# Kernel optimization log

Measured on AMD Instinct MI355X. Metric: run time of the kernel, lower is better.

## Reference

```python
import jax, jax.numpy as jnp
import numpy as np

NEG_SLOPE = 0.2  # HANConv default negative_slope
N_NODES = 100000
N_REL = 8
N_EDGES = 200000
N_LABEL = 131072
C_IN = 128
H1 = 128
H2 = 128


def _segment_softmax(logits, seg, num_segments):
    # PyG softmax(src, index): exp(src - max_per_seg) / (sum_per_seg + 1e-16)
    m = jax.ops.segment_max(logits, seg, num_segments=num_segments)
    m = jnp.where(jnp.isfinite(m), m, 0.0)  # empty segments -> 0
    e = jnp.exp(logits - m[seg])
    s = jax.ops.segment_sum(e, seg, num_segments=num_segments)
    return e / (s[seg] + 1e-16)


def _han_layer(x, edge_index, proj_w, proj_b, att_src, att_dst, q, klin_w, klin_b):
    # x: [N, Cin]; edge_index: [R, 2, E]; att_src/att_dst: [R, D]; klin_w: [D, D] (torch [out,in])
    N = x.shape[0]
    h = x @ proj_w + proj_b            # [N, D] shared projection for node type 'node'
    a_src = h @ att_src.T              # [N, R] per-node src attention logits
    a_dst = h @ att_dst.T              # [N, R]

    def per_rel(eidx, a_s, a_d):
        src, dst = eidx[0], eidx[1]
        alpha = jax.nn.leaky_relu(a_s[src] + a_d[dst], NEG_SLOPE)     # [E]
        alpha = _segment_softmax(alpha, dst, N)                        # softmax over in-neighbors
        out = jax.ops.segment_sum(alpha[:, None] * h[src], dst, num_segments=N)  # [N, D]
        return jax.nn.relu(out)        # HANConv applies relu per edge-type output

    outs = jax.vmap(per_rel, in_axes=(0, 1, 1))(edge_index, a_src, a_dst)  # [R, N, D]
    # semantic attention across edge types (group())
    score = jnp.einsum('d,rd->r', q, jnp.tanh(outs @ klin_w.T + klin_b).mean(axis=1))
    attn = jax.nn.softmax(score)       # [R]
    return jnp.einsum('r,rnd->nd', attn, outs)


def setup_inputs() -> dict:
    key = jax.random.key(0)
    ks = jax.random.split(key, 24)
    f32 = jnp.float32

    def lin_w(k, fin, fout):
        return (jax.random.normal(k, (fin, fout), f32) / np.sqrt(fin)).astype(f32)

    inp = {
        'x': jax.random.normal(ks[0], (N_NODES, C_IN), f32),
        'edge_index': jax.random.randint(ks[1], (N_REL, 2, N_EDGES), 0, N_NODES, jnp.int32),
        'edge_label_index': jax.random.randint(ks[2], (2, N_LABEL), 0, N_NODES, jnp.int32),
        # HANConv layer 1 params
        'w1': lin_w(ks[3], C_IN, H1), 'b1': jnp.zeros((H1,), f32),
        'asrc1': jax.random.normal(ks[4], (N_REL, H1), f32) / np.sqrt(H1),
        'adst1': jax.random.normal(ks[5], (N_REL, H1), f32) / np.sqrt(H1),
        'q1': jax.random.normal(ks[6], (H1,), f32) / np.sqrt(H1),
        'kw1': lin_w(ks[7], H1, H1).T, 'kb1': jnp.zeros((H1,), f32),
        # HANConv layer 2 params
        'w2': lin_w(ks[8], H1, H2), 'b2': jnp.zeros((H2,), f32),
        'asrc2': jax.random.normal(ks[9], (N_REL, H2), f32) / np.sqrt(H2),
        'adst2': jax.random.normal(ks[10], (N_REL, H2), f32) / np.sqrt(H2),
        'q2': jax.random.normal(ks[11], (H2,), f32) / np.sqrt(H2),
        'kw2': lin_w(ks[12], H2, H2).T, 'kb2': jnp.zeros((H2,), f32),
        # link-score head
        'post_w': lin_w(ks[13], H2, 2), 'post_b': jnp.zeros((2,), f32),
    }
    return inp


def reference(x, edge_index, edge_label_index,
              w1, b1, asrc1, adst1, q1, kw1, kb1,
              w2, b2, asrc2, adst2, q2, kw2, kb2,
              post_w, post_b):
    h = jax.nn.relu(_han_layer(x, edge_index, w1, b1, asrc1, adst1, q1, kw1, kb1))
    h = jax.nn.relu(_han_layer(h, edge_index, w2, b2, asrc2, adst2, q2, kw2, kb2))
    h_had = h[edge_label_index[0]] * h[edge_label_index[1]]   # [L, H2]
    logits = h_had @ post_w + post_b                          # [L, 2]
    return logits.sum(axis=-1)                                # [L]
```

## Files before the change

kernel.cpp:

```cpp
#include <hip/hip_runtime.h>

#define NN 100000
#define NR 8
#define NE 200000
#define NL 131072
#define NSEG (NR*NN)
#define NB_SCAN 782
#define NPAD (NB_SCAN*1024)

typedef __attribute__((ext_vector_type(8))) short short8;
typedef __attribute__((ext_vector_type(4))) float floatx4;

__device__ __forceinline__ unsigned short f2bf(float f) {
    unsigned u = __float_as_uint(f);
    unsigned r = (u + 0x7fff + ((u >> 16) & 1)) >> 16;
    return (unsigned short)r;
}
__device__ __forceinline__ float bf2f(unsigned short s) {
    return __uint_as_float(((unsigned)s) << 16);
}

__global__ void transpose128(const float* __restrict__ in, float* __restrict__ out) {
    int idx = blockIdx.x * 256 + threadIdx.x;
    int j = idx >> 7, k = idx & 127;
    out[idx] = in[k * 128 + j];
}

__global__ void cast_bf16(const float* __restrict__ src, unsigned short* __restrict__ dst) {
    size_t idx = ((size_t)blockIdx.x * 256 + threadIdx.x) * 4;
    float4 v = *(const float4*)(src + idx);
    ushort4 o;
    o.x = f2bf(v.x); o.y = f2bf(v.y); o.z = f2bf(v.z); o.w = f2bf(v.w);
    *(ushort4*)(dst + idx) = o;
}

__global__ void hist_kernel(const int* __restrict__ ei, int* __restrict__ counts) {
    int idx = blockIdx.x * 256 + threadIdx.x;
    if (idx >= NR * NE) return;
    int r = idx / NE, e = idx - r * NE;
    int dst = ei[(size_t)r * 2 * NE + NE + e];
    atomicAdd(&counts[r * NN + dst], 1);
}

__global__ __launch_bounds__(256) void scan_k1(const int* __restrict__ counts,
                                               int* __restrict__ rowptr,
                                               int* __restrict__ bsums) {
    __shared__ int wsum[4];
    int t = threadIdx.x, lane = t & 63, w = t >> 6;
    int base = blockIdx.x * 1024 + t * 4;
    int c0 = counts[base], c1 = counts[base + 1], c2 = counts[base + 2], c3 = counts[base + 3];
    int s = c0 + c1 + c2 + c3;
    int inc = s;
#pragma unroll
    for (int off = 1; off < 64; off <<= 1) { int v = __shfl_up(inc, off); if (lane >= off) inc += v; }
    if (lane == 63) wsum[w] = inc;
    __syncthreads();
    int wbase = 0;
    for (int k = 0; k < w; ++k) wbase += wsum[k];
    int ex = wbase + inc - s;
    rowptr[base]     = ex;
    rowptr[base + 1] = ex + c0;
    rowptr[base + 2] = ex + c0 + c1;
    rowptr[base + 3] = ex + c0 + c1 + c2;
    if (t == 255) bsums[blockIdx.x] = wbase + inc;
}

__global__ __launch_bounds__(256) void scan_k2(int* __restrict__ bsums, int nb) {
    __shared__ int wsum[4];
    __shared__ int carry_s;
    int t = threadIdx.x, lane = t & 63, w = t >> 6;
    if (t == 0) carry_s = 0;
    __syncthreads();
    for (int base = 0; base < nb; base += 256) {
        int i = base + t;
        int v = (i < nb) ? bsums[i] : 0;
        int inc = v;
#pragma unroll
        for (int off = 1; off < 64; off <<= 1) { int u = __shfl_up(inc, off); if (lane >= off) inc += u; }
        if (lane == 63) wsum[w] = inc;
        __syncthreads();
        int wbase = carry_s;
        for (int k = 0; k < w; ++k) wbase += wsum[k];
        if (i < nb) bsums[i] = wbase + inc - v;
        __syncthreads();
        if (t == 0) carry_s += wsum[0] + wsum[1] + wsum[2] + wsum[3];
        __syncthreads();
    }
}

__global__ void scan_k3(int* __restrict__ rowptr, const int* __restrict__ bsums) {
    int i = blockIdx.x * 256 + threadIdx.x;
    if (i <= NSEG) rowptr[i] += bsums[i >> 10];
}

__global__ void fill_kernel(const int* __restrict__ ei, const int* __restrict__ rowptr,
                            int* __restrict__ cursor, int* __restrict__ es_raw) {
    int idx = blockIdx.x * 256 + threadIdx.x;
    if (idx >= NR * NE) return;
    int r = idx / NE, e = idx - r * NE;
    int src = ei[(size_t)r * 2 * NE + e];
    int dst = ei[(size_t)r * 2 * NE + NE + e];
    int g = r * NN + dst;
    int pos = rowptr[g] + atomicAdd(&cursor[g], 1);
    es_raw[2 * pos] = src;
}

__global__ __launch_bounds__(256, 3) void gemm_proj(
    const float* __restrict__ A, const float* __restrict__ B,
    const float* __restrict__ bias, float* __restrict__ out, int nrows)
{
    __shared__ float As[128][36];
    __shared__ float Bs[128][36];
    const int tid = threadIdx.x;
    const int row0 = blockIdx.x * 128;
    const int cg = tid & 15;
    const int nb = (tid >> 4) * 8;

    float acc[8][8];
#pragma unroll
    for (int i = 0; i < 8; ++i)
#pragma unroll
        for (int j = 0; j < 8; ++j) acc[i][j] = 0.f;

    for (int k0 = 0; k0 < 128; k0 += 32) {
#pragma unroll
        for (int i = 0; i < 4; ++i) {
            int fi = tid + i * 256;
            int rw = fi >> 3, kq = fi & 7;
            int n = row0 + rw;
            float4 v = make_float4(0.f, 0.f, 0.f, 0.f);
            if (n < nrows) v = *(const float4*)(A + (size_t)n * 128 + k0 + kq * 4);
            *(float4*)&As[rw][kq * 4] = v;
            float4 w = *(const float4*)(B + rw * 128 + k0 + kq * 4);
            *(float4*)&Bs[rw][kq * 4] = w;
        }
        __syncthreads();
#pragma unroll 2
        for (int kq = 0; kq < 8; ++kq) {
            float4 wv[8];
#pragma unroll
            for (int j = 0; j < 8; ++j) wv[j] = *(const float4*)&Bs[cg + 16 * j][kq * 4];
#pragma unroll
            for (int i = 0; i < 8; ++i) {
                float4 xv = *(const float4*)&As[nb + i][kq * 4];
#pragma unroll
                for (int j = 0; j < 8; ++j)
                    acc[i][j] += xv.x * wv[j].x + xv.y * wv[j].y
                               + xv.z * wv[j].z + xv.w * wv[j].w;
            }
        }
        __syncthreads();
    }
#pragma unroll
    for (int i = 0; i < 8; ++i) {
        int n = row0 + nb + i;
        if (n < nrows) {
#pragma unroll
            for (int j = 0; j < 8; ++j) {
                int d = cg + 16 * j;
                out[(size_t)n * 128 + d] = acc[i][j] + bias[d];
            }
        }
    }
}

__global__ __launch_bounds__(256) void fused_score2(
    const int* __restrict__ rowptr, const int2* __restrict__ es,
    const unsigned short* __restrict__ h16,
    const unsigned short* __restrict__ kw16, const float* __restrict__ kb,
    const float* __restrict__ q, float* __restrict__ scorebuf)
{
    __shared__ unsigned short Os[64][136];
    __shared__ float redbuf[4];
    const int t = threadIdx.x;
    const int r = blockIdx.y;
    const int row0 = blockIdx.x * 64;
    const int l = t & 7, ng = t >> 3;

#pragma unroll
    for (int pass = 0; pass < 2; ++pass) {
        int nl = pass * 32 + ng;
        int n = row0 + nl;
        float acc[16];
#pragma unroll
        for (int i = 0; i < 16; ++i) acc[i] = 0.f;
        if (n < NN) {
            int g = r * NN + n;
            int p0 = rowptr[g], p1 = rowptr[g + 1];
            int e = p0;
            for (; e + 1 < p1; e += 2) {
                int2 ea = es[e], eb = es[e + 1];
                float aa = __int_as_float(ea.y), ab = __int_as_float(eb.y);
                const unsigned short* hpa = h16 + (size_t)ea.x * 128;
                const unsigned short* hpb = h16 + (size_t)eb.x * 128;
                short8 a0 = *(const short8*)(hpa + l * 8);
                short8 a1 = *(const short8*)(hpa + 64 + l * 8);
                short8 b0 = *(const short8*)(hpb + l * 8);
                short8 b1 = *(const short8*)(hpb + 64 + l * 8);
#pragma unroll
                for (int i = 0; i < 8; ++i)
                    acc[i]     += aa * bf2f((unsigned short)a0[i]) + ab * bf2f((unsigned short)b0[i]);
#pragma unroll
                for (int i = 0; i < 8; ++i)
                    acc[8 + i] += aa * bf2f((unsigned short)a1[i]) + ab * bf2f((unsigned short)b1[i]);
            }
            if (e < p1) {
                int2 ea = es[e];
                float aa = __int_as_float(ea.y);
                const unsigned short* hpa = h16 + (size_t)ea.x * 128;
                short8 a0 = *(const short8*)(hpa + l * 8);
                short8 a1 = *(const short8*)(hpa + 64 + l * 8);
#pragma unroll
                for (int i = 0; i < 8; ++i) acc[i]     += aa * bf2f((unsigned short)a0[i]);
#pragma unroll
                for (int i = 0; i < 8; ++i) acc[8 + i] += aa * bf2f((unsigned short)a1[i]);
            }
        }
        unsigned short ov[16];
#pragma unroll
        for (int i = 0; i < 16; ++i) ov[i] = f2bf(fmaxf(acc[i], 0.f));
        *(short8*)&Os[nl][l * 8]      = *(short8*)&ov[0];
        *(short8*)&Os[nl][64 + l * 8] = *(short8*)&ov[8];
    }
    __syncthreads();

    const int wave = t >> 6, lane = t & 63;
    const int quad = lane >> 4, l16 = lane & 15;
    short8 a[4];
#pragma unroll
    for (int kc = 0; kc < 4; ++kc)
        a[kc] = *(const short8*)&Os[wave * 16 + l16][quad * 8 + kc * 32];

    float s = 0.f;
#pragma unroll
    for (int dt = 0; dt < 8; ++dt) {
        const unsigned short* brow = kw16 + (size_t)(dt * 16 + l16) * 128 + quad * 8;
        floatx4 accv = {0.f, 0.f, 0.f, 0.f};
#pragma unroll
        for (int kc = 0; kc < 4; ++kc) {
            short8 b = *(const short8*)(brow + kc * 32);
            accv = __builtin_amdgcn_mfma_f32_16x16x32_bf16(a[kc], b, accv, 0, 0, 0);
        }
        int d = dt * 16 + l16;
        float kbv = kb[d], qv = q[d];
#pragma unroll
        for (int reg = 0; reg < 4; ++reg) {
            int node = row0 + wave * 16 + quad * 4 + reg;
            if (node < NN) {
                float y = accv[reg] + kbv;
                float e2 = __expf(2.f * y);
                float tn = 1.f - 2.f * __builtin_amdgcn_rcpf(e2 + 1.f);
                s += tn * qv;
            }
        }
    }
    for (int off = 32; off > 0; off >>= 1) s += __shfl_down(s, off);
    if (lane == 0) redbuf[wave] = s;
    __syncthreads();
    if (t == 0) atomicAdd(scorebuf + r * 64 + (blockIdx.x & 63),
                          redbuf[0] + redbuf[1] + redbuf[2] + redbuf[3]);
}

__global__ void score_reduce(const float* __restrict__ scorebuf, float* __restrict__ score) {
    int t = threadIdx.x;
    int r = t >> 3, k = t & 7;
    float v = 0.f;
#pragma unroll
    for (int i = 0; i < 8; ++i) v += scorebuf[r * 64 + k * 8 + i];
    v += __shfl_down(v, 4);
    v += __shfl_down(v, 2);
    v += __shfl_down(v, 1);
    if (k == 0) score[r] = v;
}

__global__ __launch_bounds__(256) void att_kernel(
    const float* __restrict__ h, const float* __restrict__ asrc_w,
    const float* __restrict__ adst_w, float* __restrict__ a_src,
    float* __restrict__ a_dst, unsigned short* __restrict__ h16)
{
    __shared__ float hs[16][128];
    int n0 = blockIdx.x * 16;
#pragma unroll
    for (int i = 0; i < 2; ++i) {
        int fi = threadIdx.x + i * 256;
        int n = fi >> 5, kq = fi & 31;
        float4 v = make_float4(0.f, 0.f, 0.f, 0.f);
        if (n0 + n < NN) v = *(const float4*)(h + (size_t)(n0 + n) * 128 + kq * 4);
        *(float4*)&hs[n][kq * 4] = v;
    }
    __syncthreads();
    int n = threadIdx.x >> 4, rr = threadIdx.x & 15;
    int r = rr & 7; int isd = rr >> 3;
    const float* w = (isd ? adst_w : asrc_w) + r * 128;
    float acc = 0.f;
#pragma unroll
    for (int kq = 0; kq < 32; ++kq) {
        float4 hv = *(const float4*)&hs[n][kq * 4];
        float4 wv = ((const float4*)w)[kq];
        acc += hv.x * wv.x + hv.y * wv.y + hv.z * wv.z + hv.w * wv.w;
    }
    if (n0 + n < NN) (isd ? a_dst : a_src)[r * NN + n0 + n] = acc;

    int dq = rr * 8;
    if (n0 + n < NN) {
        unsigned short ov[8];
#pragma unroll
        for (int k = 0; k < 8; ++k) ov[k] = f2bf(hs[n][dq + k]);
        *(short8*)(h16 + (size_t)(n0 + n) * 128 + dq) = *(short8*)ov;
    }
}

__global__ void softmax_csr(const int* __restrict__ rowptr, int2* __restrict__ es,
                            const float* __restrict__ a_src, const float* __restrict__ a_dst)
{
    int g = blockIdx.x * 256 + threadIdx.x;
    if (g >= NSEG) return;
    int p0 = rowptr[g], p1 = rowptr[g + 1];
    if (p0 == p1) return;
    int r = g / NN;
    float ad = a_dst[g];
    const float* as = a_src + (size_t)r * NN;
    float m = -1e30f;
    int i = p0;
    for (; i + 1 < p1; i += 2) {
        float la = as[es[i].x] + ad;
        float lb = as[es[i + 1].x] + ad;
        la = la > 0.f ? la : 0.2f * la;
        lb = lb > 0.f ? lb : 0.2f * lb;
        es[i].y     = __float_as_int(la);
        es[i + 1].y = __float_as_int(lb);
        m = fmaxf(m, fmaxf(la, lb));
    }
    if (i < p1) {
        float la = as[es[i].x] + ad;
        la = la > 0.f ? la : 0.2f * la;
        es[i].y = __float_as_int(la);
        m = fmaxf(m, la);
    }
    float s = 0.f;
    for (int k = p0; k < p1; ++k) {
        float e = __expf(__int_as_float(es[k].y) - m);
        es[k].y = __float_as_int(e);
        s += e;
    }
    float inv = __builtin_amdgcn_rcpf(s + 1e-16f);
    for (int k = p0; k < p1; ++k)
        es[k].y = __float_as_int(__int_as_float(es[k].y) * inv);
}

__global__ __launch_bounds__(256) void combine_csr(
    const int* __restrict__ rowptr, const int2* __restrict__ es,
    const float* __restrict__ h, const float* __restrict__ score,
    float* __restrict__ comb)
{
    __shared__ float attn[NR];
    __shared__ float lds[4][64][17];
    int t = threadIdx.x;
    if (t == 0) {
        float sc[NR]; float m = -1e30f;
        for (int r = 0; r < NR; ++r) { sc[r] = score[r] * (1.0f / NN); m = fmaxf(m, sc[r]); }
        float den = 0.f;
        for (int r = 0; r < NR; ++r) { sc[r] = __expf(sc[r] - m); den += sc[r]; }
        for (int r = 0; r < NR; ++r) attn[r] = sc[r] / den;
    }
    __syncthreads();

    int nl = t >> 6;
    int n = blockIdx.x * 4 + nl;
    int L = t & 63;
    int r = L >> 3;
    int o = L & 7;
    float a[16];
#pragma unroll
    for (int i = 0; i < 16; ++i) a[i] = 0.f;
    {
        int g = r * NN + n;
        int p0 = rowptr[g], p1 = rowptr[g + 1];
        int e = p0;
        for (; e + 1 < p1; e += 2) {
            int2 ea = es[e], eb = es[e + 1];
            float aa = __int_as_float(ea.y), ab = __int_as_float(eb.y);
            const float* hpa = h + (size_t)ea.x * 128 + o * 4;
            const float* hpb = h + (size_t)eb.x * 128 + o * 4;
            float4 u0 = *(const float4*)hpa,        u1 = *(const float4*)(hpa + 32);
            float4 u2 = *(const float4*)(hpa + 64), u3 = *(const float4*)(hpa + 96);
            float4 v0 = *(const float4*)hpb,        v1 = *(const float4*)(hpb + 32);
            float4 v2 = *(const float4*)(hpb + 64), v3 = *(const float4*)(hpb + 96);
            a[0] += aa*u0.x + ab*v0.x; a[1] += aa*u0.y + ab*v0.y;
            a[2] += aa*u0.z + ab*v0.z; a[3] += aa*u0.w + ab*v0.w;
            a[4] += aa*u1.x + ab*v1.x; a[5] += aa*u1.y + ab*v1.y;
            a[6] += aa*u1.z + ab*v1.z; a[7] += aa*u1.w + ab*v1.w;
            a[8] += aa*u2.x + ab*v2.x; a[9] += aa*u2.y + ab*v2.y;
            a[10]+= aa*u2.z + ab*v2.z; a[11]+= aa*u2.w + ab*v2.w;
            a[12]+= aa*u3.x + ab*v3.x; a[13]+= aa*u3.y + ab*v3.y;
            a[14]+= aa*u3.z + ab*v3.z; a[15]+= aa*u3.w + ab*v3.w;
        }
        if (e < p1) {
            int2 ea = es[e];
            float aa = __int_as_float(ea.y);
            const float* hpa = h + (size_t)ea.x * 128 + o * 4;
            float4 u0 = *(const float4*)hpa,        u1 = *(const float4*)(hpa + 32);
            float4 u2 = *(const float4*)(hpa + 64), u3 = *(const float4*)(hpa + 96);
            a[0] += aa*u0.x; a[1] += aa*u0.y; a[2] += aa*u0.z;  a[3] += aa*u0.w;
            a[4] += aa*u1.x; a[5] += aa*u1.y; a[6] += aa*u1.z;  a[7] += aa*u1.w;
            a[8] += aa*u2.x; a[9] += aa*u2.y; a[10]+= aa*u2.z;  a[11]+= aa*u2.w;
            a[12]+= aa*u3.x; a[13]+= aa*u3.y; a[14]+= aa*u3.z;  a[15]+= aa*u3.w;
        }
    }
    float w = attn[r];
    float* dst = &lds[nl][L][0];
#pragma unroll
    for (int i = 0; i < 16; ++i) dst[i] = w * fmaxf(a[i], 0.f);
    __syncthreads();

    int o2 = L >> 3, j = L & 7;
    float s0 = 0.f, s1 = 0.f;
#pragma unroll
    for (int rr = 0; rr < NR; ++rr) {
        s0 += lds[nl][rr * 8 + o2][2 * j];
        s1 += lds[nl][rr * 8 + o2][2 * j + 1];
    }
    int d0 = ((2 * j) >> 2) * 32 + o2 * 4 + ((2 * j) & 3);
    *(float2*)(comb + (size_t)n * 128 + d0) = make_float2(s0, s1);
}

__global__ __launch_bounds__(256) void head_kernel(
    const float* __restrict__ hfin, const int* __restrict__ eli,
    const float* __restrict__ pw, const float* __restrict__ pb,
    float* __restrict__ out)
{
    int t = threadIdx.x;
    int l = blockIdx.x * 4 + (t >> 6);
    int d0 = (t & 63) * 2;
    int a = eli[l], b = eli[NL + l];
    float2 ha = *(const float2*)(hfin + (size_t)a * 128 + d0);
    float2 hb = *(const float2*)(hfin + (size_t)b * 128 + d0);
    float w0 = pw[d0 * 2] + pw[d0 * 2 + 1];
    float w1 = pw[d0 * 2 + 2] + pw[d0 * 2 + 3];
    float v = ha.x * hb.x * w0 + ha.y * hb.y * w1;
    for (int off = 32; off > 0; off >>= 1) v += __shfl_down(v, off);
    if ((t & 63) == 0) out[l] = v + pb[0] + pb[1];
}

extern "C" void kernel_launch(void* const* d_in, const int* in_sizes, int n_in,
                              void* d_out, int out_size, void* d_ws, size_t ws_size,
                              hipStream_t stream)
{
    const float* x     = (const float*)d_in[0];
    const int*   ei    = (const int*)d_in[1];
    const int*   eli   = (const int*)d_in[2];
    const float* w1    = (const float*)d_in[3];
    const float* b1    = (const float*)d_in[4];
    const float* asrc1 = (const float*)d_in[5];
    const float* adst1 = (const float*)d_in[6];
    const float* q1    = (const float*)d_in[7];
    const float* kw1   = (const float*)d_in[8];
    const float* kb1   = (const float*)d_in[9];
    const float* w2    = (const float*)d_in[10];
    const float* b2    = (const float*)d_in[11];
    const float* asrc2 = (const float*)d_in[12];
    const float* adst2 = (const float*)d_in[13];
    const float* q2    = (const float*)d_in[14];
    const float* kw2   = (const float*)d_in[15];
    const float* kb2   = (const float*)d_in[16];
    const float* pw    = (const float*)d_in[17];
    const float* pb    = (const float*)d_in[18];
    float* out = (float*)d_out;

    float* ws      = (float*)d_ws;
    float* hA      = ws;
    float* hB      = ws + 12800000ull;
    float* a_src   = ws + 25600000ull;
    float* a_dst   = ws + 26400000ull;
    int2*  es      = (int2*)(ws + 27200000ull);
    int*   rowptr  = (int*)(ws + 30400000ull);
    int*   counts  = (int*)(ws + 31200768ull);
    int*   bsums   = (int*)(ws + 32001536ull);
    float* score   = ws + 32002560ull;
    float* wt      = ws + 32002624ull;
    unsigned short* kw16 = (unsigned short*)(ws + 32019008ull);
    float* scorebuf = (float*)counts;
    unsigned short* h16 = (unsigned short*)hB;

    hipMemsetAsync(counts, 0, NPAD * sizeof(int), stream);
    hist_kernel<<<6250, 256, 0, stream>>>(ei, counts);
    scan_k1<<<NB_SCAN, 256, 0, stream>>>(counts, rowptr, bsums);
    scan_k2<<<1, 256, 0, stream>>>(bsums, NB_SCAN);
    scan_k3<<<3126, 256, 0, stream>>>(rowptr, bsums);
    hipMemsetAsync(counts, 0, NPAD * sizeof(int), stream);
    fill_kernel<<<6250, 256, 0, stream>>>(ei, rowptr, counts, (int*)es);

    for (int layer = 0; layer < 2; ++layer) {
        const float* Ain  = layer ? hB : x;
        const float* W    = layer ? w2 : w1;
        const float* bb   = layer ? b2 : b1;
        const float* as_w = layer ? asrc2 : asrc1;
        const float* ad_w = layer ? adst2 : adst1;
        const float* qq   = layer ? q2 : q1;
        const float* kw   = layer ? kw2 : kw1;
        const float* kb   = layer ? kb2 : kb1;

        transpose128<<<64, 256, 0, stream>>>(W, wt);
        gemm_proj<<<782, 256, 0, stream>>>(Ain, wt, bb, hA, NN);
        cast_bf16<<<16, 256, 0, stream>>>(kw, kw16);
        att_kernel<<<6250, 256, 0, stream>>>(hA, as_w, ad_w, a_src, a_dst, h16);
        softmax_csr<<<3125, 256, 0, stream>>>(rowptr, es, a_src, a_dst);
        hipMemsetAsync(scorebuf, 0, 512 * sizeof(float), stream);
        fused_score2<<<dim3(1563, NR), 256, 0, stream>>>(rowptr, es, h16,
                                                         kw16, kb, qq, scorebuf);
        score_reduce<<<1, 64, 0, stream>>>(scorebuf, score);
        combine_csr<<<25000, 256, 0, stream>>>(rowptr, es, hA, score, hB);
    }
    head_kernel<<<32768, 256, 0, stream>>>(hB, eli, pw, pb, out);
}
```

Before: 1.391 ms.

## Materialize per-relation outputs in fused_score2 and combine them densely

When the workspace is large enough, fused_score2 now writes each relation's ReLU'd fp32 aggregation to a dense buffer (relation 0 reuses hA) with nontemporal stores. A new combine_dense kernel then forms the attention-weighted sum with streaming reads, instead of combine_csr re-gathering neighbour rows through the CSR. This replaces random row gathers with sequential traffic, but adds about 400 MB of writes and reads per layer and needs a much larger workspace. The old path remains as a fallback.

```diff
diff --git a/kernel.cpp b/kernel.cpp
--- a/kernel.cpp
+++ b/kernel.cpp
@@ -168,7 +168,8 @@
     const int* __restrict__ rowptr, const int2* __restrict__ es,
     const unsigned short* __restrict__ h16,
     const unsigned short* __restrict__ kw16, const float* __restrict__ kb,
-    const float* __restrict__ q, float* __restrict__ scorebuf)
+    const float* __restrict__ q, float* __restrict__ scorebuf,
+    float* __restrict__ O0, float* __restrict__ Oext)
 {
     __shared__ unsigned short Os[64][136];
     __shared__ float redbuf[4];
@@ -176,6 +177,7 @@
     const int r = blockIdx.y;
     const int row0 = blockIdx.x * 64;
     const int l = t & 7, ng = t >> 3;
+    float* Orel = O0 ? ((r == 0) ? O0 : Oext + (size_t)(r - 1) * NN * 128) : nullptr;
 
 #pragma unroll
     for (int pass = 0; pass < 2; ++pass) {
@@ -216,9 +218,23 @@
                 for (int i = 0; i < 8; ++i) acc[8 + i] += aa * bf2f((unsigned short)a1[i]);
             }
         }
+        float rl[16];
+#pragma unroll
+        for (int i = 0; i < 16; ++i) rl[i] = fmaxf(acc[i], 0.f);
+        if (Orel && n < NN) {
+            float* orow = Orel + (size_t)n * 128;
+            floatx4 s0 = {rl[0], rl[1], rl[2], rl[3]};
+            floatx4 s1 = {rl[4], rl[5], rl[6], rl[7]};
+            floatx4 s2 = {rl[8], rl[9], rl[10], rl[11]};
+            floatx4 s3 = {rl[12], rl[13], rl[14], rl[15]};
+            __builtin_nontemporal_store(s0, (floatx4*)(orow + l * 8));
+            __builtin_nontemporal_store(s1, (floatx4*)(orow + l * 8 + 4));
+            __builtin_nontemporal_store(s2, (floatx4*)(orow + 64 + l * 8));
+            __builtin_nontemporal_store(s3, (floatx4*)(orow + 64 + l * 8 + 4));
+        }
         unsigned short ov[16];
 #pragma unroll
-        for (int i = 0; i < 16; ++i) ov[i] = f2bf(fmaxf(acc[i], 0.f));
+        for (int i = 0; i < 16; ++i) ov[i] = f2bf(rl[i]);
         *(short8*)&Os[nl][l * 8]      = *(short8*)&ov[0];
         *(short8*)&Os[nl][64 + l * 8] = *(short8*)&ov[8];
     }
@@ -346,6 +362,40 @@
     float inv = __builtin_amdgcn_rcpf(s + 1e-16f);
     for (int k = p0; k < p1; ++k)
         es[k].y = __float_as_int(__int_as_float(es[k].y) * inv);
+}
+
+__global__ __launch_bounds__(256) void combine_dense(
+    const float* __restrict__ O0, const float* __restrict__ Oext,
+    const float* __restrict__ score, float* __restrict__ comb)
+{
+    __shared__ float attn[NR];
+    int t = threadIdx.x;
+    if (t == 0) {
+        float sc[NR]; float m = -1e30f;
+        for (int r = 0; r < NR; ++r) { sc[r] = score[r] * (1.0f / NN); m = fmaxf(m, sc[r]); }
+        float den = 0.f;
+        for (int r = 0; r < NR; ++r) { sc[r] = __expf(sc[r] - m); den += sc[r]; }
+        for (int r = 0; r < NR; ++r) attn[r] = sc[r] / den;
+    }
+    __syncthreads();
+    float w[NR];
+#pragma unroll
+    for (int r = 0; r < NR; ++r) w[r] = attn[r];
+
+    const size_t total = (size_t)NN * 32;
+    const size_t rstride = (size_t)NN * 32;
+    for (size_t i = (size_t)blockIdx.x * 256 + t; i < total;
+         i += (size_t)gridDim.x * 256) {
+        floatx4 v = __builtin_nontemporal_load((const floatx4*)O0 + i);
+        floatx4 a = w[0] * v;
+#pragma unroll
+        for (int r = 1; r < NR; ++r) {
+            floatx4 u = __builtin_nontemporal_load(
+                (const floatx4*)Oext + (size_t)(r - 1) * rstride + i);
+            a += w[r] * u;
+        }
+        ((floatx4*)comb)[i] = a;
+    }
 }
 
 __global__ __launch_bounds__(256) void combine_csr(
@@ -479,6 +529,8 @@
     float* score   = ws + 32002560ull;
     float* wt      = ws + 32002624ull;
     unsigned short* kw16 = (unsigned short*)(ws + 32019008ull);
+    float* Oext    = ws + 32027200ull;
+    const bool bigws = ws_size >= 121627200ull * sizeof(float);
     float* scorebuf = (float*)counts;
     unsigned short* h16 = (unsigned short*)hB;
 
@@ -507,9 +559,14 @@
         softmax_csr<<<3125, 256, 0, stream>>>(rowptr, es, a_src, a_dst);
         hipMemsetAsync(scorebuf, 0, 512 * sizeof(float), stream);
         fused_score2<<<dim3(1563, NR), 256, 0, stream>>>(rowptr, es, h16,
-                                                         kw16, kb, qq, scorebuf);
+                                                         kw16, kb, qq, scorebuf,
+                                                         bigws ? hA : nullptr,
+                                                         bigws ? Oext : nullptr);
         score_reduce<<<1, 64, 0, stream>>>(scorebuf, score);
-        combine_csr<<<25000, 256, 0, stream>>>(rowptr, es, hA, score, hB);
+        if (bigws)
+            combine_dense<<<2048, 256, 0, stream>>>(hA, Oext, score, hB);
+        else
+            combine_csr<<<25000, 256, 0, stream>>>(rowptr, es, hA, score, hB);
     }
     head_kernel<<<32768, 256, 0, stream>>>(hB, eli, pw, pb, out);
 }
```

Measured after the change: 1.405 ms. Within noise of the previous version (+1.0%).
